# Performance work log

Hardware: AMD Instinct MI355X
Metric: run time of the kernel (lower is better)

The kernel has to match this reference:

```python
import jax, jax.numpy as jnp
import numpy as np

WS = 7          # window size (7x7)
N = WS * WS     # tokens per window = 49
C = 192         # channels
H = 6           # heads
NW = 64         # windows per image (for mask)
B_ = 8192       # num_windows * batch


def _rel_index():
    coords = np.stack(np.meshgrid(np.arange(WS), np.arange(WS), indexing='ij'))  # [2,7,7]
    cf = coords.reshape(2, -1)                       # [2,49]
    rc = (cf[:, :, None] - cf[:, None, :]).transpose(1, 2, 0).astype(np.int64)  # [49,49,2]
    rc[..., 0] += WS - 1
    rc[..., 1] += WS - 1
    rc[..., 0] *= 2 * WS - 1
    return jnp.asarray(rc.sum(-1), dtype=jnp.int32)  # [49,49], values in [0, 169)


def setup_inputs() -> dict:
    key = jax.random.key(0)
    ks = jax.random.split(key, 10)
    std = 0.02
    return {
        'xq': jax.random.normal(ks[0], (B_, N, C), dtype=jnp.float32),
        'mask': jax.random.normal(ks[1], (NW, N, N), dtype=jnp.float32),
        'Wq': jax.random.normal(ks[2], (C, C), dtype=jnp.float32) * std,
        'bq': jnp.zeros((C,), dtype=jnp.float32),
        'Wkv': jax.random.normal(ks[3], (C, 2 * C), dtype=jnp.float32) * std,
        'bkv': jnp.zeros((2 * C,), dtype=jnp.float32),
        'Wproj': jax.random.normal(ks[4], (C, C), dtype=jnp.float32) * std,
        'bproj': jnp.zeros((C,), dtype=jnp.float32),
        'bias_table': jax.random.normal(ks[5], ((2 * WS - 1) * (2 * WS - 1), H), dtype=jnp.float32) * std,
        'rel_index': _rel_index(),
    }


def reference(xq, mask, Wq, bq, Wkv, bkv, Wproj, bproj, bias_table, rel_index):
    b_, n, c = xq.shape
    h = H
    dh = c // h
    scale = dh ** (-0.5)
    # projections (xkv = xq since xkv is None in the original call)
    q = (xq @ Wq + bq).reshape(b_, n, h, dh).transpose(0, 2, 1, 3) * scale      # [b_,h,n,dh]
    kv = (xq @ Wkv + bkv).reshape(b_, n, 2, h, dh).transpose(2, 0, 3, 1, 4)     # [2,b_,h,n,dh]
    k, v = kv[0], kv[1]
    attn = jnp.einsum('bhqd,bhkd->bhqk', q, k)                                   # [b_,h,n,n]
    # gathered relative-position bias: [n,n,h] -> [h,n,n]
    bias = bias_table[rel_index.reshape(-1)].reshape(n, n, h).transpose(2, 0, 1)
    attn = attn + bias[None]
    # mask add: [b_//nw, nw, h, n, n] + [1, nw, 1, n, n]
    nw = mask.shape[0]
    attn = attn.reshape(b_ // nw, nw, h, n, n) + mask[None, :, None]
    attn = jax.nn.softmax(attn.reshape(b_, h, n, n), axis=-1)
    x = jnp.einsum('bhqk,bhkd->bhqd', attn, v).transpose(0, 2, 1, 3).reshape(b_, n, c)
    return x @ Wproj + bproj
```

## Files before the change

### kernel.cpp

```cpp
#include <hip/hip_runtime.h>


#define NTOK 49
#define CCH 192

typedef __bf16 bf16_t;
typedef bf16_t bf16x8 __attribute__((ext_vector_type(8)));
typedef bf16_t bf16x4 __attribute__((ext_vector_type(4)));
typedef bf16_t bf16x2 __attribute__((ext_vector_type(2)));
typedef float f32x4 __attribute__((ext_vector_type(4)));

#define WS_WQT   0
#define WS_WKVT  73728
#define WS_WPT   221184
#define WS_BQS   294912
#define WS_TBL   295680

#define SWZ(row, off) ((off) ^ (((row) & 7) << 4))

__device__ __forceinline__ unsigned pk2(float a, float b) {
    bf16x2 w = { (bf16_t)a, (bf16_t)b };
    return __builtin_bit_cast(unsigned, w);
}

__global__ void prep_kernel(const float* __restrict__ Wq, const float* __restrict__ bq,
                            const float* __restrict__ Wkv, const float* __restrict__ Wproj,
                            const float* __restrict__ btab, const int* __restrict__ rel,
                            const float* __restrict__ mask,
                            bf16_t* __restrict__ wqt, bf16_t* __restrict__ wkvt,
                            bf16_t* __restrict__ wpt, float* __restrict__ bqs,
                            float* __restrict__ tbl, int mode) {
    const float SC  = 0.2550718212080052f;
    const float L2E = 1.4426950408889634f;
    long i = (long)blockIdx.x * 256 + threadIdx.x;
    if (i < 36864) { int n = i / 192, k = i % 192; wqt[i] = (bf16_t)(Wq[k * 192 + n] * SC); return; }
    i -= 36864;
    if (i < 73728) { int n = i / 192, k = i % 192; wkvt[i] = (bf16_t)Wkv[k * 384 + n]; return; }
    i -= 73728;
    if (i < 36864) { int n = i / 192, k = i % 192; wpt[i] = (bf16_t)Wproj[k * 192 + n]; return; }
    i -= 36864;
    if (i < 192) { bqs[i] = bq[i] * SC; return; }
    i -= 192;
    if (mode == 0) {
        if (i < 1204224) {
            int c = i & 63; long r = i >> 6; int q = r % 49; r /= 49; int h = r % 6; int w = r / 6;
            tbl[i] = (c < 49) ? (btab[rel[q * 49 + c] * 6 + h] + mask[(size_t)w * 2401 + q * 49 + c]) * L2E
                              : -1e30f;
        }
    } else if (mode == 1) {
        if (i < 18816) { int c = i & 63; int r = i >> 6; int q = r % 49; int h = r / 49;
            tbl[i] = (c < 49) ? btab[rel[q * 49 + c] * 6 + h] * L2E : 0.f; return; }
        i -= 18816;
        if (i < 200704) { int c = i & 63; long r = i >> 6; int q = r % 49; int w = r / 49;
            tbl[18816 + i] = (c < 49) ? mask[(size_t)w * 2401 + q * 49 + c] * L2E : -1e30f; }
    } else {
        if (i < 14406) { int h = i / 2401, rc = i % 2401; tbl[i] = btab[rel[rc] * 6 + h]; }
    }
}

__global__ __launch_bounds__(512, 4) void wattn_kernel(
    const float* __restrict__ xq, const float* __restrict__ mask,
    const float* __restrict__ bkv, const float* __restrict__ bproj,
    const bf16_t* __restrict__ wqt, const bf16_t* __restrict__ wkvt, const bf16_t* __restrict__ wpt,
    const float* __restrict__ bqs, const float* __restrict__ tbl,
    float* __restrict__ out, int mode)
{
    __shared__ __align__(16) unsigned char smem[73728];
    unsigned char* QsO = smem;
    unsigned char* Ks  = smem + 24576;
    unsigned char* Vt  = smem + 49152;

    const int tid = threadIdx.x;
    const int wid = tid >> 6;
    const int lane = tid & 63;
    const int l15 = lane & 15;
    const int lg = lane >> 4;
    const int t0 = blockIdx.x;
    const int b = (t0 & 0x1FC0) | ((t0 & 7) << 3) | ((t0 >> 3) & 7);
    const float* xp = xq + (size_t)b * (NTOK * CCH);
    const float LOG2E = 1.4426950408889634f;

    const int mtp = wid & 1;
    const int ntq = wid >> 1;
    bf16x8 xf[2][6];
#pragma unroll
    for (int e = 0; e < 2; e++) {
        int tok = (mtp * 2 + e) * 16 + l15;
        const float* xrow = xp + (size_t)tok * 192;
        bool ok = (tok < NTOK);
#pragma unroll
        for (int ks = 0; ks < 6; ks++) {
            float4 a = { 0.f, 0.f, 0.f, 0.f }, c = { 0.f, 0.f, 0.f, 0.f };
            if (ok) {
                a = *(const float4*)(xrow + ks * 32 + lg * 8);
                c = *(const float4*)(xrow + ks * 32 + lg * 8 + 4);
            }
            bf16x8 f = { (bf16_t)a.x, (bf16_t)a.y, (bf16_t)a.z, (bf16_t)a.w,
                         (bf16_t)c.x, (bf16_t)c.y, (bf16_t)c.z, (bf16_t)c.w };
            xf[e][ks] = f;
        }
    }
    for (int k9 = 0; k9 < 9; k9++) {
        int nt = ntq + 4 * k9;
        int kind = nt < 12 ? 0 : (nt < 24 ? 1 : 2);
        int ncol = (nt - (kind == 1 ? 12 : (kind == 2 ? 24 : 0))) * 16;
        const bf16_t* wr;
        if (kind == 0)      wr = wqt  + (size_t)(ncol + l15) * 192 + lg * 8;
        else if (kind == 1) wr = wkvt + (size_t)(ncol + l15) * 192 + lg * 8;
        else                wr = wkvt + (size_t)(192 + ncol + l15) * 192 + lg * 8;
        bf16x8 bfr[6];
#pragma unroll
        for (int ks = 0; ks < 6; ks++) bfr[ks] = *(const bf16x8*)(wr + ks * 32);

        if (kind < 2) {
            float4 b4 = (kind == 0) ? *(const float4*)(bqs + ncol + lg * 4)
                                    : *(const float4*)(bkv + ncol + lg * 4);
            f32x4 acc0 = { b4.x, b4.y, b4.z, b4.w }, acc1 = acc0;
#pragma unroll
            for (int ks = 0; ks < 6; ks++) {
                acc0 = __builtin_amdgcn_mfma_f32_16x16x32_bf16(bfr[ks], xf[0][ks], acc0, 0, 0, 0);
                acc1 = __builtin_amdgcn_mfma_f32_16x16x32_bf16(bfr[ks], xf[1][ks], acc1, 0, 0, 0);
            }
            unsigned char* dst = (kind == 0) ? QsO : Ks;
            int tr0 = (mtp * 2) * 16 + l15;
            int tr1 = tr0 + 16;
            bf16x4 p0 = { (bf16_t)acc0[0], (bf16_t)acc0[1], (bf16_t)acc0[2], (bf16_t)acc0[3] };
            bf16x4 p1 = { (bf16_t)acc1[0], (bf16_t)acc1[1], (bf16_t)acc1[2], (bf16_t)acc1[3] };
            *(bf16x4*)(dst + tr0 * 384 + SWZ(tr0, ncol * 2 + lg * 8)) = p0;
            *(bf16x4*)(dst + tr1 * 384 + SWZ(tr1, ncol * 2 + lg * 8)) = p1;
        } else {
            float bv = bkv[192 + ncol + l15];
            f32x4 acc0 = { bv, bv, bv, bv }, acc1 = acc0;
#pragma unroll
            for (int ks = 0; ks < 6; ks++) {
                acc0 = __builtin_amdgcn_mfma_f32_16x16x32_bf16(xf[0][ks], bfr[ks], acc0, 0, 0, 0);
                acc1 = __builtin_amdgcn_mfma_f32_16x16x32_bf16(xf[1][ks], bfr[ks], acc1, 0, 0, 0);
            }
            int vr = ncol + l15;
            bf16x4 v0 = { (bf16_t)acc0[0], (bf16_t)acc0[1], (bf16_t)acc0[2], (bf16_t)acc0[3] };
            bf16x4 v1 = { (bf16_t)acc1[0], (bf16_t)acc1[1], (bf16_t)acc1[2], (bf16_t)acc1[3] };
            *(bf16x4*)(Vt + vr * 128 + SWZ(vr, (mtp * 2) * 32 + lg * 8)) = v0;
            *(bf16x4*)(Vt + vr * 128 + SWZ(vr, (mtp * 2 + 1) * 32 + lg * 8)) = v1;
        }
    }
    __syncthreads();

    const int widx = b & 63;
    for (int i3 = 0; i3 < 3; i3++) {
        int u = wid + 8 * i3;
        int h = u >> 2, qtl = u & 3;
        int qrow = qtl * 16 + l15;
        bf16x8 qfr = *(const bf16x8*)(QsO + qrow * 384 + SWZ(qrow, h * 64 + lg * 16));
        f32x4 s[4];
#pragma unroll
        for (int f = 0; f < 4; f++) {
            int kr = f * 16 + l15;
            bf16x8 kfr = *(const bf16x8*)(Ks + kr * 384 + SWZ(kr, h * 64 + lg * 16));
            f32x4 z = { 0.f, 0.f, 0.f, 0.f };
            s[f] = __builtin_amdgcn_mfma_f32_16x16x32_bf16(kfr, qfr, z, 0, 0, 0);
        }
        int q = qtl * 16 + l15;
        bool qok = (q < NTOK);
        if (mode == 0) {
#pragma unroll
            for (int f = 0; f < 4; f++) {
                if (qok) {
                    float4 bm = *(const float4*)(tbl + (((size_t)(widx * 6 + h) * 49 + q) << 6) + f * 16 + lg * 4);
                    s[f][0] += bm.x; s[f][1] += bm.y; s[f][2] += bm.z; s[f][3] += bm.w;
                }
            }
        } else if (mode == 1) {
#pragma unroll
            for (int f = 0; f < 4; f++) {
                if (qok) {
                    float4 b1 = *(const float4*)(tbl + (((size_t)(h * 49 + q)) << 6) + f * 16 + lg * 4);
                    float4 m1 = *(const float4*)(tbl + 18816 + (((size_t)(widx * 49 + q)) << 6) + f * 16 + lg * 4);
                    s[f][0] += b1.x + m1.x; s[f][1] += b1.y + m1.y;
                    s[f][2] += b1.z + m1.z; s[f][3] += b1.w + m1.w;
                }
            }
        } else {
#pragma unroll
            for (int f = 0; f < 4; f++)
#pragma unroll
                for (int j = 0; j < 4; j++) {
                    int k = f * 16 + lg * 4 + j;
                    if (k >= NTOK) s[f][j] = -1e30f;
                    else if (qok)
                        s[f][j] += (tbl[h * 2401 + q * 49 + k] + mask[(size_t)widx * 2401 + q * 49 + k]) * LOG2E;
                }
        }
        float m = s[0][0];
#pragma unroll
        for (int f = 0; f < 4; f++)
#pragma unroll
            for (int j = 0; j < 4; j++) m = fmaxf(m, s[f][j]);
        m = fmaxf(m, __shfl_xor(m, 16));
        m = fmaxf(m, __shfl_xor(m, 32));
        float t = 0.f;
#pragma unroll
        for (int f = 0; f < 4; f++)
#pragma unroll
            for (int j = 0; j < 4; j++) { s[f][j] = __builtin_amdgcn_exp2f(s[f][j] - m); t += s[f][j]; }
        t += __shfl_xor(t, 16);
        t += __shfl_xor(t, 32);
        float inv = __builtin_amdgcn_rcpf(t);
        unsigned Wp[8];
#pragma unroll
        for (int f = 0; f < 4; f++) {
            Wp[f * 2 + 0] = pk2(s[f][0], s[f][1]);
            Wp[f * 2 + 1] = pk2(s[f][2], s[f][3]);
        }
        bf16x8 pa[2];
#pragma unroll
        for (int ks2 = 0; ks2 < 2; ks2++) {
            unsigned pw[4];
#pragma unroll
            for (int p = 0; p < 4; p++) {
                int src = l15 + 16 * (((lg & 1) << 1) | (p >> 1));
                unsigned v0 = (unsigned)__shfl((int)Wp[(2 * ks2) * 2 + (p & 1)], src, 64);
                unsigned v1 = (unsigned)__shfl((int)Wp[(2 * ks2 + 1) * 2 + (p & 1)], src, 64);
                pw[p] = (lg & 2) ? v1 : v0;
            }
            uint4 pp = { pw[0], pw[1], pw[2], pw[3] };
            pa[ks2] = __builtin_bit_cast(bf16x8, pp);
        }
#pragma unroll
        for (int dt = 0; dt < 2; dt++) {
            f32x4 acc = { 0.f, 0.f, 0.f, 0.f };
#pragma unroll
            for (int ks2 = 0; ks2 < 2; ks2++) {
                int vr = h * 32 + dt * 16 + l15;
                bf16x8 vfr = *(const bf16x8*)(Vt + vr * 128 + SWZ(vr, ks2 * 64 + lg * 16));
                acc = __builtin_amdgcn_mfma_f32_16x16x32_bf16(vfr, pa[ks2], acc, 0, 0, 0);
            }
            int orow = qtl * 16 + l15;
            bf16x4 op4 = { (bf16_t)(acc[0] * inv), (bf16_t)(acc[1] * inv),
                           (bf16_t)(acc[2] * inv), (bf16_t)(acc[3] * inv) };
            *(bf16x4*)(QsO + orow * 384 + SWZ(orow, h * 64 + dt * 32 + lg * 8)) = op4;
        }
    }
    __syncthreads();

    {
        float* op = out + (size_t)b * (NTOK * CCH);
        bf16x8 bfr[6];
        float4 b4 = { 0.f, 0.f, 0.f, 0.f };
        int prev_nt = -1;
        for (int i = 0; i < 6; i++) {
            int u = wid * 6 + i;
            int nt = u >> 2, mt = u & 3;
            if (nt != prev_nt) {
                prev_nt = nt;
                const bf16_t* wr = wpt + (size_t)(nt * 16 + l15) * 192 + lg * 8;
#pragma unroll
                for (int ks = 0; ks < 6; ks++) bfr[ks] = *(const bf16x8*)(wr + ks * 32);
                b4 = *(const float4*)(bproj + nt * 16 + lg * 4);
            }
            int orow = mt * 16 + l15;
            f32x4 acc = { b4.x, b4.y, b4.z, b4.w };
#pragma unroll
            for (int ks = 0; ks < 6; ks++) {
                bf16x8 of = *(const bf16x8*)(QsO + orow * 384 + SWZ(orow, ks * 64 + lg * 16));
                acc = __builtin_amdgcn_mfma_f32_16x16x32_bf16(bfr[ks], of, acc, 0, 0, 0);
            }
            if (orow < NTOK) {
                float4 st = { acc[0], acc[1], acc[2], acc[3] };
                *(float4*)(op + orow * 192 + nt * 16 + lg * 4) = st;
            }
        }
    }
}

extern "C" void kernel_launch(void* const* d_in, const int* in_sizes, int n_in,
                              void* d_out, int out_size, void* d_ws, size_t ws_size,
                              hipStream_t stream) {
    const float* xq    = (const float*)d_in[0];
    const float* mask  = (const float*)d_in[1];
    const float* Wq    = (const float*)d_in[2];
    const float* bq    = (const float*)d_in[3];
    const float* Wkv   = (const float*)d_in[4];
    const float* bkv   = (const float*)d_in[5];
    const float* Wproj = (const float*)d_in[6];
    const float* bproj = (const float*)d_in[7];
    const float* btab  = (const float*)d_in[8];
    const int*   rel   = (const int*)d_in[9];
    float* out = (float*)d_out;

    char* ws = (char*)d_ws;
    bf16_t* wqt  = (bf16_t*)(ws + WS_WQT);
    bf16_t* wkvt = (bf16_t*)(ws + WS_WKVT);
    bf16_t* wpt  = (bf16_t*)(ws + WS_WPT);
    float*  bqs  = (float*)(ws + WS_BQS);
    float*  tbl  = (float*)(ws + WS_TBL);

    size_t need0 = (size_t)WS_TBL + 1204224u * 4u;
    size_t need1 = (size_t)WS_TBL + 219520u * 4u;
    int mode = (ws_size >= need0) ? 0 : (ws_size >= need1 ? 1 : 2);

    long tblN = (mode == 0) ? 1204224L : (mode == 1 ? 219520L : 14406L);
    long prep_elems = 147648L + tblN;
    int prep_blocks = (int)((prep_elems + 255) / 256);
    prep_kernel<<<prep_blocks, 256, 0, stream>>>(Wq, bq, Wkv, Wproj, btab, rel, mask,
                                                 wqt, wkvt, wpt, bqs, tbl, mode);
    wattn_kernel<<<8192, 512, 0, stream>>>(xq, mask, bkv, bproj, wqt, wkvt, wpt,
                                           bqs, tbl, out, mode);
}
```

Before: 736.9 us.

## Split fused window attention into separate QKV projection and attention kernels

Splits the single fused kernel into two. The first computes the Q/K/V projections and writes them to a bf16 workspace buffer; the second loads them, runs masked softmax attention and the output projection. The split is meant to give each stage lower register and LDS pressure and better occupancy, and the attention kernel also prefetches bias/mask rows one iteration ahead. The cost is an extra global round trip of about 56 KB per window, and the path only runs when the workspace is large enough, chunking over windows otherwise.

```diff
diff --git a/kernel.cpp b/kernel.cpp
--- a/kernel.cpp
+++ b/kernel.cpp
@@ -15,6 +15,9 @@
 #define WS_WPT   221184
 #define WS_BQS   294912
 #define WS_TBL   295680
+#define WS_QKV   5112576
+#define QKV_ELEMS_PER_WIN 28224
+#define QKV_BYTES_PER_WIN 56448
 
 #define SWZ(row, off) ((off) ^ (((row) & 7) << 4))
 
@@ -58,7 +61,278 @@
     }
 }
 
-__global__ __launch_bounds__(512, 4) void wattn_kernel(
+__global__ __launch_bounds__(512, 4) void qkv_kernel(
+    const float* __restrict__ xq, const float* __restrict__ bkv,
+    const bf16_t* __restrict__ wqt, const bf16_t* __restrict__ wkvt,
+    const float* __restrict__ bqs, bf16_t* __restrict__ qkv, int base)
+{
+    const int tid = threadIdx.x;
+    const int wid = tid >> 6;
+    const int lane = tid & 63;
+    const int l15 = lane & 15;
+    const int lg = lane >> 4;
+    const int b = base + blockIdx.x;
+    const float* xp = xq + (size_t)b * (NTOK * CCH);
+    bf16_t* og = qkv + (size_t)blockIdx.x * QKV_ELEMS_PER_WIN;
+
+    const int mtp = wid & 1;
+    const int ntq = wid >> 1;
+    bf16x8 xf[2][6];
+#pragma unroll
+    for (int e = 0; e < 2; e++) {
+        int tok = (mtp * 2 + e) * 16 + l15;
+        const float* xrow = xp + (size_t)tok * 192;
+        bool ok = (tok < NTOK);
+#pragma unroll
+        for (int ks = 0; ks < 6; ks++) {
+            float4 a = { 0.f, 0.f, 0.f, 0.f }, c = { 0.f, 0.f, 0.f, 0.f };
+            if (ok) {
+                a = *(const float4*)(xrow + ks * 32 + lg * 8);
+                c = *(const float4*)(xrow + ks * 32 + lg * 8 + 4);
+            }
+            bf16x8 f = { (bf16_t)a.x, (bf16_t)a.y, (bf16_t)a.z, (bf16_t)a.w,
+                         (bf16_t)c.x, (bf16_t)c.y, (bf16_t)c.z, (bf16_t)c.w };
+            xf[e][ks] = f;
+        }
+    }
+    for (int k9 = 0; k9 < 9; k9++) {
+        int nt = ntq + 4 * k9;
+        int kind = nt < 12 ? 0 : (nt < 24 ? 1 : 2);
+        int ncol = (nt - (kind == 1 ? 12 : (kind == 2 ? 24 : 0))) * 16;
+        int wofs = (kind == 2) ? 192 : 0;
+        const bf16_t* wr = (kind == 0) ? (wqt + (size_t)(ncol + l15) * 192 + lg * 8)
+                                       : (wkvt + (size_t)(wofs + ncol + l15) * 192 + lg * 8);
+        float4 b4 = (kind == 0) ? *(const float4*)(bqs + ncol + lg * 4)
+                                : *(const float4*)(bkv + wofs + ncol + lg * 4);
+        bf16x8 bfr[6];
+#pragma unroll
+        for (int ks = 0; ks < 6; ks++) bfr[ks] = *(const bf16x8*)(wr + ks * 32);
+        f32x4 acc0 = { b4.x, b4.y, b4.z, b4.w }, acc1 = acc0;
+#pragma unroll
+        for (int ks = 0; ks < 6; ks++) {
+            acc0 = __builtin_amdgcn_mfma_f32_16x16x32_bf16(bfr[ks], xf[0][ks], acc0, 0, 0, 0);
+            acc1 = __builtin_amdgcn_mfma_f32_16x16x32_bf16(bfr[ks], xf[1][ks], acc1, 0, 0, 0);
+        }
+        bf16_t* dstb = og + (kind == 0 ? 0 : (kind == 1 ? 9408 : 18816));
+        int tr0 = mtp * 32 + l15;
+        int tr1 = tr0 + 16;
+        bf16x4 p0 = { (bf16_t)acc0[0], (bf16_t)acc0[1], (bf16_t)acc0[2], (bf16_t)acc0[3] };
+        bf16x4 p1 = { (bf16_t)acc1[0], (bf16_t)acc1[1], (bf16_t)acc1[2], (bf16_t)acc1[3] };
+        if (tr0 < NTOK) *(bf16x4*)(dstb + (size_t)tr0 * 192 + ncol + lg * 4) = p0;
+        if (tr1 < NTOK) *(bf16x4*)(dstb + (size_t)tr1 * 192 + ncol + lg * 4) = p1;
+    }
+}
+
+__global__ __launch_bounds__(512, 4) void attn_kernel(
+    const bf16_t* __restrict__ qkv, const float* __restrict__ mask,
+    const bf16_t* __restrict__ wpt, const float* __restrict__ bproj,
+    const float* __restrict__ tbl, float* __restrict__ out, int base, int mode)
+{
+    __shared__ __align__(16) unsigned char smem[73728];
+    unsigned char* Ks = smem;
+    unsigned char* Vt = smem + 24576;
+    unsigned char* Os = smem + 49152;
+
+    const int tid = threadIdx.x;
+    const int wid = tid >> 6;
+    const int lane = tid & 63;
+    const int l15 = lane & 15;
+    const int lg = lane >> 4;
+    const int t0 = blockIdx.x;
+    const int bl = (t0 & ~63) | ((t0 & 7) << 3) | ((t0 >> 3) & 7);
+    const int b = base + bl;
+    const int widx = b & 63;
+    const float LOG2E = 1.4426950408889634f;
+
+    const bf16_t* qg = qkv + (size_t)bl * QKV_ELEMS_PER_WIN;
+    const bf16_t* kg = qg + 9408;
+    const bf16_t* vg = qg + 18816;
+
+    for (int idx = tid; idx < 1176; idx += 512) {
+        int row = idx / 24, c8 = (idx % 24) * 8;
+        bf16x8 v = *(const bf16x8*)(kg + (size_t)row * 192 + c8);
+        *(bf16x8*)(Ks + row * 384 + SWZ(row, c8 * 2)) = v;
+    }
+    if (tid < 512) {
+        for (int idx = tid; idx < 720; idx += 512)
+            *(unsigned long long*)(Ks + 49 * 384 + idx * 8) = 0ULL;
+    }
+    for (int idx = tid; idx < 1176; idx += 512) {
+        int row = idx / 24, c8 = (idx % 24) * 8;
+        bf16x8 v = *(const bf16x8*)(vg + (size_t)row * 192 + c8);
+#pragma unroll
+        for (int e = 0; e < 8; e++)
+            *(bf16_t*)(Vt + (c8 + e) * 128 + SWZ(c8 + e, row * 2)) = v[e];
+    }
+    for (int idx = tid; idx < 2880; idx += 512) {
+        int ch = idx / 15, tc = 49 + idx % 15;
+        *(bf16_t*)(Vt + ch * 128 + SWZ(ch, tc * 2)) = (bf16_t)0.f;
+    }
+    uint4 zz = { 0u, 0u, 0u, 0u };
+    bf16x8 qf[3];
+#pragma unroll
+    for (int i3 = 0; i3 < 3; i3++) {
+        int u = wid + 8 * i3, h = u >> 2, qtl = u & 3;
+        int qrow = qtl * 16 + l15;
+        qf[i3] = (qrow < NTOK) ? *(const bf16x8*)(qg + (size_t)qrow * 192 + h * 32 + lg * 8)
+                               : __builtin_bit_cast(bf16x8, zz);
+    }
+    float4 tb0[4], tb1[4];
+    auto tload = [&](int i3, float4* dst) {
+        int u = wid + 8 * i3, h = u >> 2, qtl = u & 3;
+        int q = qtl * 16 + l15;
+        if (q < NTOK) {
+            const float* tp = tbl + (((size_t)(widx * 6 + h) * 49 + q) << 6) + lg * 4;
+#pragma unroll
+            for (int f = 0; f < 4; f++) dst[f] = *(const float4*)(tp + f * 16);
+        } else {
+#pragma unroll
+            for (int f = 0; f < 4; f++) dst[f] = make_float4(0.f, 0.f, 0.f, 0.f);
+        }
+    };
+    if (mode == 0) tload(0, tb0);
+    __syncthreads();
+
+#pragma unroll
+    for (int i3 = 0; i3 < 3; i3++) {
+        int u = wid + 8 * i3;
+        int h = u >> 2, qtl = u & 3;
+        bf16x8 qfr = qf[i3];
+        if (mode == 0 && i3 < 2) tload(i3 + 1, (i3 & 1) ? tb0 : tb1);
+        f32x4 s[4];
+#pragma unroll
+        for (int f = 0; f < 4; f++) {
+            int kr = f * 16 + l15;
+            bf16x8 kfr = *(const bf16x8*)(Ks + kr * 384 + SWZ(kr, h * 64 + lg * 16));
+            f32x4 z = { 0.f, 0.f, 0.f, 0.f };
+            s[f] = __builtin_amdgcn_mfma_f32_16x16x32_bf16(kfr, qfr, z, 0, 0, 0);
+        }
+        int q = qtl * 16 + l15;
+        bool qok = (q < NTOK);
+        if (mode == 0) {
+            const float4* tbc = (i3 & 1) ? tb1 : tb0;
+#pragma unroll
+            for (int f = 0; f < 4; f++) {
+                if (qok) { s[f][0] += tbc[f].x; s[f][1] += tbc[f].y; s[f][2] += tbc[f].z; s[f][3] += tbc[f].w; }
+                else {
+#pragma unroll
+                    for (int j = 0; j < 4; j++) { int k = f * 16 + lg * 4 + j; if (k >= NTOK) s[f][j] = -1e30f; }
+                }
+            }
+            if (qok) {  }
+        } else if (mode == 1) {
+#pragma unroll
+            for (int f = 0; f < 4; f++) {
+                if (qok) {
+                    float4 b1 = *(const float4*)(tbl + (((size_t)(h * 49 + q)) << 6) + f * 16 + lg * 4);
+                    float4 m1 = *(const float4*)(tbl + 18816 + (((size_t)(widx * 49 + q)) << 6) + f * 16 + lg * 4);
+                    s[f][0] += b1.x + m1.x; s[f][1] += b1.y + m1.y;
+                    s[f][2] += b1.z + m1.z; s[f][3] += b1.w + m1.w;
+                } else {
+#pragma unroll
+                    for (int j = 0; j < 4; j++) { int k = f * 16 + lg * 4 + j; if (k >= NTOK) s[f][j] = -1e30f; }
+                }
+            }
+        } else {
+#pragma unroll
+            for (int f = 0; f < 4; f++)
+#pragma unroll
+                for (int j = 0; j < 4; j++) {
+                    int k = f * 16 + lg * 4 + j;
+                    if (k >= NTOK) s[f][j] = -1e30f;
+                    else if (qok)
+                        s[f][j] += (tbl[h * 2401 + q * 49 + k] + mask[(size_t)widx * 2401 + q * 49 + k]) * LOG2E;
+                }
+        }
+        if (mode == 0 && !qok) {
+#pragma unroll
+            for (int f = 0; f < 4; f++)
+#pragma unroll
+                for (int j = 0; j < 4; j++) { int k = f * 16 + lg * 4 + j; if (k >= NTOK) s[f][j] = -1e30f; }
+        }
+        float m = s[0][0];
+#pragma unroll
+        for (int f = 0; f < 4; f++)
+#pragma unroll
+            for (int j = 0; j < 4; j++) m = fmaxf(m, s[f][j]);
+        m = fmaxf(m, __shfl_xor(m, 16));
+        m = fmaxf(m, __shfl_xor(m, 32));
+        float t = 0.f;
+#pragma unroll
+        for (int f = 0; f < 4; f++)
+#pragma unroll
+            for (int j = 0; j < 4; j++) { s[f][j] = __builtin_amdgcn_exp2f(s[f][j] - m); t += s[f][j]; }
+        t += __shfl_xor(t, 16);
+        t += __shfl_xor(t, 32);
+        float inv = __builtin_amdgcn_rcpf(t);
+        unsigned Wp[8];
+#pragma unroll
+        for (int f = 0; f < 4; f++) {
+            Wp[f * 2 + 0] = pk2(s[f][0], s[f][1]);
+            Wp[f * 2 + 1] = pk2(s[f][2], s[f][3]);
+        }
+        bf16x8 pa[2];
+#pragma unroll
+        for (int ks2 = 0; ks2 < 2; ks2++) {
+            unsigned pw[4];
+#pragma unroll
+            for (int p = 0; p < 4; p++) {
+                int src = l15 + 16 * (((lg & 1) << 1) | (p >> 1));
+                unsigned v0 = (unsigned)__shfl((int)Wp[(2 * ks2) * 2 + (p & 1)], src, 64);
+                unsigned v1 = (unsigned)__shfl((int)Wp[(2 * ks2 + 1) * 2 + (p & 1)], src, 64);
+                pw[p] = (lg & 2) ? v1 : v0;
+            }
+            uint4 pp = { pw[0], pw[1], pw[2], pw[3] };
+            pa[ks2] = __builtin_bit_cast(bf16x8, pp);
+        }
+#pragma unroll
+        for (int dt = 0; dt < 2; dt++) {
+            f32x4 acc = { 0.f, 0.f, 0.f, 0.f };
+#pragma unroll
+            for (int ks2 = 0; ks2 < 2; ks2++) {
+                int vr = h * 32 + dt * 16 + l15;
+                bf16x8 vfr = *(const bf16x8*)(Vt + vr * 128 + SWZ(vr, ks2 * 64 + lg * 16));
+                acc = __builtin_amdgcn_mfma_f32_16x16x32_bf16(vfr, pa[ks2], acc, 0, 0, 0);
+            }
+            int orow = qtl * 16 + l15;
+            bf16x4 op4 = { (bf16_t)(acc[0] * inv), (bf16_t)(acc[1] * inv),
+                           (bf16_t)(acc[2] * inv), (bf16_t)(acc[3] * inv) };
+            *(bf16x4*)(Os + orow * 384 + SWZ(orow, h * 64 + dt * 32 + lg * 8)) = op4;
+        }
+    }
+    __syncthreads();
+
+    {
+        float* op = out + (size_t)b * (NTOK * CCH);
+        bf16x8 bfr[6];
+        float4 b4 = { 0.f, 0.f, 0.f, 0.f };
+        int prev_nt = -1;
+        for (int i = 0; i < 6; i++) {
+            int u = wid * 6 + i;
+            int nt = u >> 2, mt = u & 3;
+            if (nt != prev_nt) {
+                prev_nt = nt;
+                const bf16_t* wr = wpt + (size_t)(nt * 16 + l15) * 192 + lg * 8;
+#pragma unroll
+                for (int ks = 0; ks < 6; ks++) bfr[ks] = *(const bf16x8*)(wr + ks * 32);
+                b4 = *(const float4*)(bproj + nt * 16 + lg * 4);
+            }
+            int orow = mt * 16 + l15;
+            f32x4 acc = { b4.x, b4.y, b4.z, b4.w };
+#pragma unroll
+            for (int ks = 0; ks < 6; ks++) {
+                bf16x8 of = *(const bf16x8*)(Os + orow * 384 + SWZ(orow, ks * 64 + lg * 16));
+                acc = __builtin_amdgcn_mfma_f32_16x16x32_bf16(bfr[ks], of, acc, 0, 0, 0);
+            }
+            if (orow < NTOK) {
+                float4 st = { acc[0], acc[1], acc[2], acc[3] };
+                *(float4*)(op + orow * 192 + nt * 16 + lg * 4) = st;
+            }
+        }
+    }
+}
+
+__global__ __launch_bounds__(512, 4) void wattn_mono(
     const float* __restrict__ xq, const float* __restrict__ mask,
     const float* __restrict__ bkv, const float* __restrict__ bproj,
     const bf16_t* __restrict__ wqt, const bf16_t* __restrict__ wkvt, const bf16_t* __restrict__ wpt,
@@ -111,7 +385,6 @@
         bf16x8 bfr[6];
 #pragma unroll
         for (int ks = 0; ks < 6; ks++) bfr[ks] = *(const bf16x8*)(wr + ks * 32);
-
         if (kind < 2) {
             float4 b4 = (kind == 0) ? *(const float4*)(bqs + ncol + lg * 4)
                                     : *(const float4*)(bkv + ncol + lg * 4);
@@ -167,6 +440,9 @@
                 if (qok) {
                     float4 bm = *(const float4*)(tbl + (((size_t)(widx * 6 + h) * 49 + q) << 6) + f * 16 + lg * 4);
                     s[f][0] += bm.x; s[f][1] += bm.y; s[f][2] += bm.z; s[f][3] += bm.w;
+                } else {
+#pragma unroll
+                    for (int j = 0; j < 4; j++) { int k = f * 16 + lg * 4 + j; if (k >= NTOK) s[f][j] = -1e30f; }
                 }
             }
         } else if (mode == 1) {
@@ -177,6 +453,9 @@
                     float4 m1 = *(const float4*)(tbl + 18816 + (((size_t)(widx * 49 + q)) << 6) + f * 16 + lg * 4);
                     s[f][0] += b1.x + m1.x; s[f][1] += b1.y + m1.y;
                     s[f][2] += b1.z + m1.z; s[f][3] += b1.w + m1.w;
+                } else {
+#pragma unroll
+                    for (int j = 0; j < 4; j++) { int k = f * 16 + lg * 4 + j; if (k >= NTOK) s[f][j] = -1e30f; }
                 }
             }
         } else {
@@ -303,6 +582,20 @@
     int prep_blocks = (int)((prep_elems + 255) / 256);
     prep_kernel<<<prep_blocks, 256, 0, stream>>>(Wq, bq, Wkv, Wproj, btab, rel, mask,
                                                  wqt, wkvt, wpt, bqs, tbl, mode);
-    wattn_kernel<<<8192, 512, 0, stream>>>(xq, mask, bkv, bproj, wqt, wkvt, wpt,
-                                           bqs, tbl, out, mode);
+
+    size_t avail = (ws_size > (size_t)WS_QKV) ? ws_size - (size_t)WS_QKV : 0;
+    long w_c_l = (long)(avail / QKV_BYTES_PER_WIN) & ~63L;
+    int w_c = (int)(w_c_l > 8192 ? 8192 : w_c_l);
+
+    if (w_c >= 64 && mode == 0) {
+        bf16_t* qkvb = (bf16_t*)(ws + WS_QKV);
+        for (int base = 0; base < 8192; base += w_c) {
+            int n = (8192 - base) < w_c ? (8192 - base) : w_c;
+            qkv_kernel<<<n, 512, 0, stream>>>(xq, bkv, wqt, wkvt, bqs, qkvb, base);
+            attn_kernel<<<n, 512, 0, stream>>>(qkvb, mask, wpt, bproj, tbl, out, base, mode);
+        }
+    } else {
+        wattn_mono<<<8192, 512, 0, stream>>>(xq, mask, bkv, bproj, wqt, wkvt, wpt,
+                                             bqs, tbl, out, mode);
+    }
 }
```

Measured after the change: 913.8 us. 24.0% more time.
